# Performance work log

Hardware: AMD Instinct MI355X
Metric: run time of the kernel (lower is better)

The kernel has to match this reference:

```python
import jax, jax.numpy as jnp
import numpy as np

B, C, L = 8, 512, 2048   # batch, input_dim (channels), sequence length
H = 8                    # multihead_cnt
K = 3                    # kernel_dim
DH = C // H              # per-head dim = 64
SCALE = 1.0 / float(np.sqrt(C))  # module divides by sqrt(input_dim), not sqrt(head_dim)


def _conv1d(x, w, b):
    # x: [B, C, L], w: [C_out, C_in, K], padding=1 keeps L
    y = jax.lax.conv_general_dilated(x, w, window_strides=(1,), padding=[(1, 1)],
                                     dimension_numbers=('NCH', 'OIH', 'NCH'))
    return y + b[None, :, None]


def setup_inputs() -> dict:
    key = jax.random.key(0)
    ks = jax.random.split(key, 7)
    x = jax.random.normal(ks[0], (B, C, L), dtype=jnp.float32)
    # xavier_normal_ std for Conv1d weight [C, C, K]: sqrt(2 / (fan_in + fan_out)), fan = C*K
    std = float(np.sqrt(2.0 / (C * K + C * K)))
    inp = {'x': x}
    for i in range(3):  # conv_cnt = 3 -> q, k, v convolutions
        inp[f'w{i}'] = jax.random.normal(ks[1 + 2 * i], (C, C, K), dtype=jnp.float32) * std
        inp[f'b{i}'] = jax.random.normal(ks[2 + 2 * i], (C,), dtype=jnp.float32) * 0.01
    return inp


def reference(x, w0, b0, w1, b1, w2, b2):
    # q, k, v projections via Conv1d (padding preserves length)
    q = _conv1d(x, w0, b0)  # [B, C, L]
    k = _conv1d(x, w1, b1)
    v = _conv1d(x, w2, b2)
    # torch.chunk along dim 1 == contiguous reshape into heads
    qh = q.reshape(B, H, DH, L)
    kh = k.reshape(B, H, DH, L)
    vh = v.reshape(B, H, DH, L)
    # scores = q^T k / sqrt(input_dim)  -> [B, H, L, L]
    scores = jnp.einsum('bhdl,bhdm->bhlm', qh, kh) * SCALE
    att = jax.nn.softmax(scores, axis=-1)
    # out = (att @ v^T)^T -> [B, H, DH, L]
    out = jnp.einsum('bhlm,bhdm->bhdl', att, vh)
    return out.reshape(B, C, L)
```

## Files before the change

### kernel.cpp

```cpp
#include <hip/hip_runtime.h>
#include <hip/hip_bf16.h>
#include <cstdint>

typedef unsigned short u16;
typedef short v8s __attribute__((ext_vector_type(8)));
typedef float v4f __attribute__((ext_vector_type(4)));
typedef u16 u16x8 __attribute__((ext_vector_type(8)));
typedef u16 u16x4 __attribute__((ext_vector_type(4)));

static constexpr int Bb = 8, Cc = 512, Ll = 2048, Hh = 8, Dh = 64;

__device__ __forceinline__ float bf2f(u16 u){
  unsigned x = ((unsigned)u) << 16; float f; __builtin_memcpy(&f, &x, 4); return f;
}
__device__ __forceinline__ u16 f2bf(float f){
  unsigned x; __builtin_memcpy(&x, &f, 4);
  x = (x + 0x7fffu + ((x >> 16) & 1u)) >> 16; return (u16)x;
}

__device__ __forceinline__ void async_cp16(const u16* g, u16* l){
  __builtin_amdgcn_global_load_lds(
      (const __attribute__((address_space(1))) unsigned int*)g,
      (__attribute__((address_space(3))) unsigned int*)l, 16, 0, 0);
}

#if __has_builtin(__builtin_amdgcn_exp2f)
#define EXP2F(x) __builtin_amdgcn_exp2f(x)
#else
#define EXP2F(x) exp2f(x)
#endif

__global__ __launch_bounds__(256) void detect_dtype(const u16* __restrict__ x, unsigned* __restrict__ flag){
  __shared__ int cnt;
  if (threadIdx.x == 0) cnt = 0;
  __syncthreads();
  int sane = 0;
  for (int i = threadIdx.x; i < 4096; i += 256){
    unsigned e = (x[2 * i] >> 7) & 0xFFu;
    sane += (e >= 90u && e <= 160u) ? 1 : 0;
  }
  atomicAdd(&cnt, sane);
  __syncthreads();
  if (threadIdx.x == 0) *flag = (cnt < 2458) ? 1u : 0u;
}

__global__ __launch_bounds__(256) void transpose_pad(const void* __restrict__ xv, const unsigned* __restrict__ flagp,
                                                     u16* __restrict__ xT){
  int b = blockIdx.z, ci0 = blockIdx.y * 64, l0 = blockIdx.x * 64;
  __shared__ u16 tb[64 * 72];
  const unsigned isf32 = *flagp;
  int t = threadIdx.x;
  int row = t >> 3, seg = t & 7;
  if (isf32){
    const float* xf = (const float*)xv;
    #pragma unroll
    for (int rnd = 0; rnd < 2; rnd++){
      int ci = row + rnd * 32;
      size_t off = ((size_t)(b * Cc + ci0 + ci)) * Ll + l0 + seg * 8;
      v4f a = *(const v4f*)(xf + off);
      v4f c4 = *(const v4f*)(xf + off + 4);
      #pragma unroll
      for (int j = 0; j < 4; j++) tb[(seg * 8 + j) * 72 + ci] = f2bf(a[j]);
      #pragma unroll
      for (int j = 0; j < 4; j++) tb[(seg * 8 + 4 + j) * 72 + ci] = f2bf(c4[j]);
    }
  } else {
    const u16* x = (const u16*)xv;
    #pragma unroll
    for (int rnd = 0; rnd < 2; rnd++){
      int ci = row + rnd * 32;
      u16x8 v = *(const u16x8*)(x + ((size_t)(b * Cc + ci0 + ci)) * Ll + l0 + seg * 8);
      #pragma unroll
      for (int j = 0; j < 8; j++) tb[(seg * 8 + j) * 72 + ci] = v[j];
    }
  }
  __syncthreads();
  #pragma unroll
  for (int rnd = 0; rnd < 2; rnd++){
    int l = row + rnd * 32;
    u16x8 v = *(const u16x8*)&tb[l * 72 + seg * 8];
    *(u16x8*)(xT + ((size_t)b * 2050 + 1 + l0 + l) * Cc + ci0 + seg * 8) = v;
  }
  if (blockIdx.x == 0 && t < 8){
    u16x8 z = {};
    *(u16x8*)(xT + ((size_t)b * 2050 + 0) * Cc + ci0 + t * 8) = z;
  }
  if (blockIdx.x == 31 && t < 8){
    u16x8 z = {};
    *(u16x8*)(xT + ((size_t)b * 2050 + 2049) * Cc + ci0 + t * 8) = z;
  }
}

__global__ __launch_bounds__(256) void pack_wb(const void* __restrict__ w0, const void* __restrict__ w1,
                                               const void* __restrict__ w2, const void* __restrict__ b0,
                                               const void* __restrict__ b1, const void* __restrict__ b2,
                                               const unsigned* __restrict__ flagp,
                                               u16* __restrict__ wp, u16* __restrict__ bb){
  int g = blockIdx.x * 256 + threadIdx.x;
  const unsigned isf32 = *flagp;
  if (g < 9 * 512 * 512){
    int ci = g & 511, co = (g >> 9) & 511, kc = g >> 18;
    int conv = kc / 3, k = kc - conv * 3;
    const void* w = (conv == 0) ? w0 : ((conv == 1) ? w1 : w2);
    size_t idx = (size_t)co * 1536 + ci * 3 + k;
    wp[g] = isf32 ? f2bf(((const float*)w)[idx]) : ((const u16*)w)[idx];
  } else {
    int g2 = g - 9 * 512 * 512;
    if (g2 < 1536){
      int conv = g2 >> 9, c = g2 & 511;
      const void* bsrc = (conv == 0) ? b0 : ((conv == 1) ? b1 : b2);
      bb[g2] = isf32 ? f2bf(((const float*)bsrc)[c]) : ((const u16*)bsrc)[c];
    }
  }
}

__global__ __launch_bounds__(256) void conv_gemm_fused(const u16* __restrict__ wp, const u16* __restrict__ xT,
                                                       const u16* __restrict__ bb, u16* __restrict__ qT,
                                                       u16* __restrict__ kT, u16* __restrict__ vN){
  int b = blockIdx.y, bx = blockIdx.x;
  int mt = bx >> 3, nt = bx & 7;
  int m0 = mt * 128, n0 = nt * 256;
  int conv = m0 >> 9;
  int co0 = m0 & 511;
  __shared__ u16 smem[17408];
  int t = threadIdx.x, wave = t >> 6, lane = t & 63, quad = lane >> 4, lid = lane & 15;
  int wm = (wave >> 1) * 64, wn = (wave & 1) * 128;
  v4f acc[4][8] = {};
  const size_t xbase = (size_t)b * 2050 * Cc;
  const u16* wbase = wp + ((size_t)(conv * 3) * 512 + co0) * 512;

  auto stageB = [&](int it, u16* buf){
    int ci0 = it << 5;
    #pragma unroll
    for (int r = 0; r < 4; r++){
      int e = (r * 256 + t) * 8;
      int row = e >> 5, cio = e & 31;
      async_cp16(xT + xbase + (size_t)(n0 + row) * 512 + ci0 + cio, buf + e);
    }
    if (t < 8){
      int hr = 256 + (t >> 2), cio = (t & 3) * 8;
      u16x8 hv = *(const u16x8*)(xT + xbase + (size_t)(n0 + hr) * 512 + ci0 + cio);
      *(u16x8*)&buf[hr * 32 + cio] = hv;
    }
  };

  stageB(0, smem);
  __syncthreads();
  for (int it = 0; it < 16; it++){
    u16* cur = smem + (it & 1) * 8256;
    if (it + 1 < 16) stageB(it + 1, smem + ((it + 1) & 1) * 8256);
    int ci0 = it << 5;
    #pragma unroll
    for (int ks = 0; ks < 3; ks++){
      v8s aF[4], bF[8];
      const u16* wks = wbase + (size_t)ks * 512 * 512;
      #pragma unroll
      for (int i = 0; i < 4; i++)
        aF[i] = *(const v8s*)(wks + (size_t)(wm + i * 16 + lid) * 512 + ci0 + quad * 8);
      #pragma unroll
      for (int j = 0; j < 8; j++)
        bF[j] = *(const v8s*)&cur[(wn + j * 16 + lid + ks) * 32 + quad * 8];
      #pragma unroll
      for (int i = 0; i < 4; i++)
        #pragma unroll
        for (int j = 0; j < 8; j++)
          acc[i][j] = __builtin_amdgcn_mfma_f32_16x16x32_bf16(aF[i], bF[j], acc[i][j], 0, 0, 0);
    }
    __syncthreads();
  }

  const float qsc = (float)(1.4426950408889634 / 22.627416997969522);
  if (conv < 2){
    u16* dst = (conv == 0) ? qT : kT;
    #pragma unroll
    for (int i = 0; i < 4; i++){
      int cog = m0 + wm + i * 16 + quad * 4;
      float bv[4];
      #pragma unroll
      for (int r = 0; r < 4; r++) bv[r] = bf2f(bb[cog + r]);
      int co = cog & 511;
      #pragma unroll
      for (int j = 0; j < 8; j++){
        int l = n0 + wn + j * 16 + lid;
        u16x4 pk;
        #pragma unroll
        for (int r = 0; r < 4; r++){
          float v = acc[i][j][r] + bv[r];
          if (conv == 0) v *= qsc;
          pk[r] = f2bf(v);
        }
        *(u16x4*)(dst + ((((size_t)b * Hh + (co >> 6)) * Ll + l) << 6) + (co & 63)) = pk;
      }
    }
  } else {
    u16* scr = smem;
    #pragma unroll
    for (int cs = 0; cs < 2; cs++){
      __syncthreads();
      #pragma unroll
      for (int i = 0; i < 4; i++){
        int cog = m0 + wm + i * 16 + quad * 4;
        float bv[4];
        #pragma unroll
        for (int r = 0; r < 4; r++) bv[r] = bf2f(bb[cog + r]);
        #pragma unroll
        for (int j = 0; j < 4; j++){
          int jj = cs * 4 + j;
          int lcl = (wave & 1) * 64 + j * 16 + lid;
          #pragma unroll
          for (int r = 0; r < 4; r++)
            scr[(wm + i * 16 + quad * 4 + r) * 136 + lcl] = f2bf(acc[i][jj][r] + bv[r]);
        }
      }
      __syncthreads();
      int row = t & 127, half = t >> 7;
      int co = co0 + row;
      size_t gb = (((size_t)b * Cc + co) << 11) + n0 + half * 128 + cs * 64;
      #pragma unroll
      for (int s = 0; s < 8; s++){
        u16x8 vv = *(const u16x8*)&scr[row * 136 + half * 64 + s * 8];
        *(u16x8*)(vN + gb + s * 8) = vv;
      }
    }
  }
}

__global__ __launch_bounds__(256) void attn_kernel(const u16* __restrict__ qT, const u16* __restrict__ kT,
                                                   const u16* __restrict__ vN, const unsigned* __restrict__ flagp,
                                                   void* __restrict__ outv){
  int bhx = blockIdx.x;
  int b = bhx >> 3, h = bhx & 7, l0 = blockIdx.y * 128;
  int t = threadIdx.x, w = t >> 6, lane = t & 63, quad = lane >> 4, lid = lane & 15;
  __shared__ u16 kls[128 * 72];
  __shared__ u16 vls[2 * 64 * 136];
  const unsigned isf32 = *flagp;
  const size_t bh = (size_t)b * Hh + h;

  int kadd[5], vadd[5];
  bool kval[5], vval[5];
  #pragma unroll
  for (int r = 0; r < 5; r++){
    int e = (r * 256 + t) * 8;
    kval[r] = e < 128 * 72;
    int slot = e / 72, off = e - slot * 72;
    int s5 = slot & 31;
    int m = (slot & ~31) | (((s5 >> 2) & 1) << 3) | (((s5 >> 3) & 1) << 4) | (((s5 >> 4) & 1) << 2) | (s5 & 3);
    kadd[r] = m * 64 + (off < 64 ? off : 0);
    vval[r] = e < 64 * 136;
    int d = e / 136, voff = e - d * 136;
    vadd[r] = d * Ll + (voff < 128 ? voff : 0);
  }
  const u16* kTb = kT + bh * Ll * 64;
  const u16* vNb = vN + ((size_t)(b * Cc + h * Dh)) * Ll;

  #pragma unroll
  for (int r = 0; r < 5; r++)
    if (kval[r]) async_cp16(kTb + kadd[r], &kls[(r * 256 + t) * 8]);
  #pragma unroll
  for (int r = 0; r < 5; r++)
    if (vval[r]) async_cp16(vNb + vadd[r], &vls[(r * 256 + t) * 8]);

  v8s qF[2][2];
  #pragma unroll
  for (int ci = 0; ci < 2; ci++)
    #pragma unroll
    for (int ks = 0; ks < 2; ks++)
      qF[ci][ks] = *(const v8s*)(qT + ((bh * Ll) + l0 + w * 32 + ci * 16 + lid) * 64 + ks * 32 + quad * 8);

  const v8s onesF = {0x3F80, 0x3F80, 0x3F80, 0x3F80, 0x3F80, 0x3F80, 0x3F80, 0x3F80};
  v4f o[2][4] = {};
  v4f o1[2] = {};
  __syncthreads();

  for (int mt = 0; mt < 16; mt++){
    v4f s[4][2][2] = {};
    #pragma unroll
    for (int ks = 0; ks < 2; ks++){
      v8s aF[4][2];
      #pragma unroll
      for (int c = 0; c < 4; c++)
        #pragma unroll
        for (int tt = 0; tt < 2; tt++)
          aF[c][tt] = *(const v8s*)&kls[(c * 32 + tt * 16 + lid) * 72 + ks * 32 + quad * 8];
      #pragma unroll
      for (int c = 0; c < 4; c++)
        #pragma unroll
        for (int tt = 0; tt < 2; tt++){
          s[c][tt][0] = __builtin_amdgcn_mfma_f32_16x16x32_bf16(aF[c][tt], qF[0][ks], s[c][tt][0], 0, 0, 0);
          s[c][tt][1] = __builtin_amdgcn_mfma_f32_16x16x32_bf16(aF[c][tt], qF[1][ks], s[c][tt][1], 0, 0, 0);
        }
    }
    __syncthreads();

    if (mt + 1 < 16){
      const u16* kt = kTb + (size_t)(mt + 1) * 128 * 64;
      const u16* vt = vNb + (mt + 1) * 128;
      u16* vdst = vls + ((mt + 1) & 1) * (64 * 136);
      #pragma unroll
      for (int r = 0; r < 5; r++)
        if (kval[r]) async_cp16(kt + kadd[r], &kls[(r * 256 + t) * 8]);
      #pragma unroll
      for (int r = 0; r < 5; r++)
        if (vval[r]) async_cp16(vt + vadd[r], &vdst[(r * 256 + t) * 8]);
    }

    const u16* vcur = vls + (mt & 1) * (64 * 136);
    #pragma unroll
    for (int c = 0; c < 4; c++){
      v8s aP[2];
      #pragma unroll
      for (int ci = 0; ci < 2; ci++){
        float p[8];
        #pragma unroll
        for (int tt = 0; tt < 2; tt++)
          #pragma unroll
          for (int r = 0; r < 4; r++)
            p[tt * 4 + r] = EXP2F(s[c][tt][ci][r]);
        unsigned u[4];
        #pragma unroll
        for (int k2 = 0; k2 < 4; k2++){
          __hip_bfloat162 hb = __float22bfloat162_rn(make_float2(p[2 * k2], p[2 * k2 + 1]));
          __builtin_memcpy(&u[k2], &hb, 4);
        }
        __builtin_memcpy(&aP[ci], u, 16);
      }
      v8s bV[4];
      #pragma unroll
      for (int df = 0; df < 4; df++)
        bV[df] = *(const v8s*)&vcur[(df * 16 + lid) * 136 + c * 32 + quad * 8];
      #pragma unroll
      for (int ci = 0; ci < 2; ci++){
        #pragma unroll
        for (int df = 0; df < 4; df++)
          o[ci][df] = __builtin_amdgcn_mfma_f32_16x16x32_bf16(aP[ci], bV[df], o[ci][df], 0, 0, 0);
        o1[ci] = __builtin_amdgcn_mfma_f32_16x16x32_bf16(aP[ci], onesF, o1[ci], 0, 0, 0);
      }
    }
    __syncthreads();
  }

  #pragma unroll
  for (int lf = 0; lf < 2; lf++){
    v4f nv;
    #pragma unroll
    for (int r = 0; r < 4; r++) nv[r] = 1.f / o1[lf][r];
    #pragma unroll
    for (int df = 0; df < 4; df++){
      int d = df * 16 + lid;
      int l = l0 + w * 32 + lf * 16 + quad * 4;
      size_t ofs = (((bh << 6) + d) << 11) + l;
      if (isf32){
        v4f st;
        #pragma unroll
        for (int r = 0; r < 4; r++) st[r] = o[lf][df][r] * nv[r];
        *(v4f*)((float*)outv + ofs) = st;
      } else {
        u16x4 pk;
        #pragma unroll
        for (int r = 0; r < 4; r++) pk[r] = f2bf(o[lf][df][r] * nv[r]);
        *(u16x4*)((u16*)outv + ofs) = pk;
      }
    }
  }
}

extern "C" void kernel_launch(void* const* d_in, const int* in_sizes, int n_in,
                              void* d_out, int out_size, void* d_ws, size_t ws_size,
                              hipStream_t stream){
  const void* x  = d_in[0];
  const void* w0 = d_in[1];
  const void* b0 = d_in[2];
  const void* w1 = d_in[3];
  const void* b1 = d_in[4];
  const void* w2 = d_in[5];
  const void* b2 = d_in[6];
  u16* ws = (u16*)d_ws;
  unsigned* flag = (unsigned*)ws;
  u16* xT = ws + 64;
  u16* wp = xT + (size_t)8 * 2050 * 512;
  u16* bb = wp + (size_t)9 * 512 * 512;
  u16* qT = bb + 1536;
  u16* kT = qT + (size_t)8 * 8 * 2048 * 64;
  u16* vN = kT + (size_t)8 * 8 * 2048 * 64;

  detect_dtype<<<1, 256, 0, stream>>>((const u16*)x, flag);
  transpose_pad<<<dim3(32, 8, 8), 256, 0, stream>>>(x, flag, xT);
  pack_wb<<<dim3(9 * 512 * 512 / 256 + 6), 256, 0, stream>>>(w0, w1, w2, b0, b1, b2, flag, wp, bb);
  conv_gemm_fused<<<dim3(96, 8), 256, 0, stream>>>(wp, xT, bb, qT, kT, vN);
  attn_kernel<<<dim3(64, 16), 256, 0, stream>>>(qT, kT, vN, flag, d_out);
}
```

Measured before the change: 311.8 us.

## Double-buffer K tiles in attention and hoist conv weight loads before staging

The attention kernel now double-buffers K in shared memory like V, issuing the next K/V tile prefetch at the start of each iteration. This removes the mid-loop barrier that separated QK^T from the prefetch, so loads overlap with both matmuls. The conv kernel loads all three kernel-tap weight fragments from global memory before issuing the next B-tile stage, giving them more time in flight at the cost of more registers. The extra K buffer doubles K LDS usage, which may lower occupancy, and dropping the barrier relies on the existing end-of-loop sync for correctness.

```diff
diff --git a/kernel.cpp b/kernel.cpp
--- a/kernel.cpp
+++ b/kernel.cpp
@@ -148,15 +148,19 @@
   __syncthreads();
   for (int it = 0; it < 16; it++){
     u16* cur = smem + (it & 1) * 8256;
+    int ci0 = it << 5;
+    v8s aF[3][4];
+    #pragma unroll
+    for (int ks = 0; ks < 3; ks++){
+      const u16* wks = wbase + (size_t)ks * 512 * 512;
+      #pragma unroll
+      for (int i = 0; i < 4; i++)
+        aF[ks][i] = *(const v8s*)(wks + (size_t)(wm + i * 16 + lid) * 512 + ci0 + quad * 8);
+    }
     if (it + 1 < 16) stageB(it + 1, smem + ((it + 1) & 1) * 8256);
-    int ci0 = it << 5;
     #pragma unroll
     for (int ks = 0; ks < 3; ks++){
-      v8s aF[4], bF[8];
-      const u16* wks = wbase + (size_t)ks * 512 * 512;
-      #pragma unroll
-      for (int i = 0; i < 4; i++)
-        aF[i] = *(const v8s*)(wks + (size_t)(wm + i * 16 + lid) * 512 + ci0 + quad * 8);
+      v8s bF[8];
       #pragma unroll
       for (int j = 0; j < 8; j++)
         bF[j] = *(const v8s*)&cur[(wn + j * 16 + lid + ks) * 32 + quad * 8];
@@ -164,7 +168,7 @@
       for (int i = 0; i < 4; i++)
         #pragma unroll
         for (int j = 0; j < 8; j++)
-          acc[i][j] = __builtin_amdgcn_mfma_f32_16x16x32_bf16(aF[i], bF[j], acc[i][j], 0, 0, 0);
+          acc[i][j] = __builtin_amdgcn_mfma_f32_16x16x32_bf16(aF[ks][i], bF[j], acc[i][j], 0, 0, 0);
     }
     __syncthreads();
   }
@@ -231,7 +235,7 @@
   int bhx = blockIdx.x;
   int b = bhx >> 3, h = bhx & 7, l0 = blockIdx.y * 128;
   int t = threadIdx.x, w = t >> 6, lane = t & 63, quad = lane >> 4, lid = lane & 15;
-  __shared__ u16 kls[128 * 72];
+  __shared__ u16 kls[2 * 128 * 72];
   __shared__ u16 vls[2 * 64 * 136];
   const unsigned isf32 = *flagp;
   const size_t bh = (size_t)b * Hh + h;
@@ -253,12 +257,20 @@
   const u16* kTb = kT + bh * Ll * 64;
   const u16* vNb = vN + ((size_t)(b * Cc + h * Dh)) * Ll;
 
-  #pragma unroll
-  for (int r = 0; r < 5; r++)
-    if (kval[r]) async_cp16(kTb + kadd[r], &kls[(r * 256 + t) * 8]);
-  #pragma unroll
-  for (int r = 0; r < 5; r++)
-    if (vval[r]) async_cp16(vNb + vadd[r], &vls[(r * 256 + t) * 8]);
+  auto stageKV = [&](int mt){
+    const u16* kt = kTb + (size_t)mt * 128 * 64;
+    const u16* vt = vNb + mt * 128;
+    u16* kdst = kls + (mt & 1) * (128 * 72);
+    u16* vdst = vls + (mt & 1) * (64 * 136);
+    #pragma unroll
+    for (int r = 0; r < 5; r++)
+      if (kval[r]) async_cp16(kt + kadd[r], &kdst[(r * 256 + t) * 8]);
+    #pragma unroll
+    for (int r = 0; r < 5; r++)
+      if (vval[r]) async_cp16(vt + vadd[r], &vdst[(r * 256 + t) * 8]);
+  };
+
+  stageKV(0);
 
   v8s qF[2][2];
   #pragma unroll
@@ -273,6 +285,10 @@
   __syncthreads();
 
   for (int mt = 0; mt < 16; mt++){
+    const u16* kcur = kls + (mt & 1) * (128 * 72);
+    const u16* vcur = vls + (mt & 1) * (64 * 136);
+    if (mt + 1 < 16) stageKV(mt + 1);
+
     v4f s[4][2][2] = {};
     #pragma unroll
     for (int ks = 0; ks < 2; ks++){
@@ -281,7 +297,7 @@
       for (int c = 0; c < 4; c++)
         #pragma unroll
         for (int tt = 0; tt < 2; tt++)
-          aF[c][tt] = *(const v8s*)&kls[(c * 32 + tt * 16 + lid) * 72 + ks * 32 + quad * 8];
+          aF[c][tt] = *(const v8s*)&kcur[(c * 32 + tt * 16 + lid) * 72 + ks * 32 + quad * 8];
       #pragma unroll
       for (int c = 0; c < 4; c++)
         #pragma unroll
@@ -290,21 +306,7 @@
           s[c][tt][1] = __builtin_amdgcn_mfma_f32_16x16x32_bf16(aF[c][tt], qF[1][ks], s[c][tt][1], 0, 0, 0);
         }
     }
-    __syncthreads();
-
-    if (mt + 1 < 16){
-      const u16* kt = kTb + (size_t)(mt + 1) * 128 * 64;
-      const u16* vt = vNb + (mt + 1) * 128;
-      u16* vdst = vls + ((mt + 1) & 1) * (64 * 136);
-      #pragma unroll
-      for (int r = 0; r < 5; r++)
-        if (kval[r]) async_cp16(kt + kadd[r], &kls[(r * 256 + t) * 8]);
-      #pragma unroll
-      for (int r = 0; r < 5; r++)
-        if (vval[r]) async_cp16(vt + vadd[r], &vdst[(r * 256 + t) * 8]);
-    }
-
-    const u16* vcur = vls + (mt & 1) * (64 * 136);
+
     #pragma unroll
     for (int c = 0; c < 4; c++){
       v8s aP[2];
```

Result: no change. 316.4 us (+1.5%).
